# Kernel optimization log

Measured on AMD Instinct MI355X. Metric: run time of the kernel, lower is better.

## Reference

```python
import jax, jax.numpy as jnp
import numpy as np

# Sizes: B graphs, NPG nodes per graph (equal segments -> to_dense_batch == reshape),
# M instructions, DN node feat dim, DQ question dim.
B, NPG, M, DN, DQ = 64, 4096, 8, 512, 256
N = B * NPG
RATIO = 0.3
K = int(np.ceil(RATIO * NPG))  # pyg topk with ratio<1 keeps ceil(ratio*n) nodes per graph


def setup_inputs() -> dict:
    key = jax.random.key(0)
    ks = jax.random.split(key, 4)
    x = jax.random.normal(ks[0], (N, DN), jnp.float32)
    u = jax.random.normal(ks[1], (M, B, DQ), jnp.float32)
    Wn = jax.random.normal(ks[2], (DN, DQ), jnp.float32) / np.sqrt(DN)
    bn = jnp.zeros((DQ,), jnp.float32)
    batch = jnp.repeat(jnp.arange(B, dtype=jnp.int32), NPG)  # sorted graph ids, equal segments
    edge_index = jax.random.randint(ks[3], (2, 4 * N), 0, N, dtype=jnp.int32)  # unused by forward
    return {"x": x, "u": u, "Wn": Wn, "bn": bn, "batch": batch, "edge_index": edge_index}


def reference(x, u, Wn, bn, batch, edge_index):
    # node_nn: Linear(DN, DQ) + exact GELU (torch.nn.GELU default)
    h = jax.nn.gelu(x @ Wn + bn, approximate=False)            # [N, DQ]
    # to_dense_batch with equal-size graphs == reshape, mask all True
    hb = h.reshape(B, NPG, DQ)                                  # [B, n, D]
    inst = jnp.transpose(u, (1, 0, 2))                          # [B, M, D]
    scores = jnp.einsum('bmd,bnd->bmn', inst, hb)               # [B, M, n]
    attn = jax.nn.softmax(scores, axis=2)
    gate = attn.sum(axis=1)                                     # [B, n]  (gate[batch_mask] flatten)
    # per-graph ratio top-k -> hard binary mask (index_fill_ 1 at top-k, 0 elsewhere)
    kth = jax.lax.top_k(gate, K)[0][:, -1:]                     # k-th largest per graph
    mask = (gate >= kth).astype(h.dtype)                        # [B, n]
    return mask.reshape(N)
```

## Files before the change

kernel.cpp:

```cpp
#include <hip/hip_runtime.h>
#include <math.h>

#define B_     64
#define NPG_   4096
#define M_     8
#define DN_    512
#define DQ_    256
#define N_     (B_*NPG_)
#define KSEL_  1229

typedef _Float16 f16x4  __attribute__((ext_vector_type(4)));
typedef _Float16 f16x8  __attribute__((ext_vector_type(8)));
typedef float    f32x16 __attribute__((ext_vector_type(16)));

__global__ __launch_bounds__(256) void k_prep(const float* __restrict__ Wn,
                                              _Float16* __restrict__ th,
                                              _Float16* __restrict__ tl)
{
    const int k = blockIdx.x;
    const int c = threadIdx.x;
    const float w = Wn[k * DQ_ + c];
    const _Float16 h = (_Float16)w;
    th[c * DN_ + k] = h;
    tl[c * DN_ + k] = (_Float16)(w - (float)h);
}

__global__ __launch_bounds__(256, 2) void k_score(
    const float* __restrict__ x, const float* __restrict__ u,
    const float* __restrict__ bn,
    const _Float16* __restrict__ wth, const _Float16* __restrict__ wtl,
    float* __restrict__ scores)
{
    __shared__ __align__(16) _Float16 Ahi[64][40],  Alo[64][40];
    __shared__ __align__(16) _Float16 Bhi[256][40], Blo[256][40];
    __shared__ float usS[M_][DQ_];
    __shared__ float bnsS[DQ_];
    float* part4f = (float*)&Bhi[0][0];

    const int tid = threadIdx.x;
    const int ln  = tid & 63;
    const int wc  = tid >> 6;
    const int lr  = ln & 31;
    const int lh  = ln >> 5;
    const int row0 = blockIdx.x * 64;
    const int b    = row0 >> 12;

    #pragma unroll
    for (int p = 0; p < 8; ++p) {
        const int idx = p * 256 + tid;
        usS[idx >> 8][idx & 255] = u[((idx >> 8) * B_ + b) * DQ_ + (idx & 255)];
    }
    bnsS[tid] = bn[tid];

    const int arow  = tid >> 2;
    const int akoff = (tid & 3) * 8;
    const float*  xp  = x + (long)(row0 + arow) * DN_ + akoff;
    const float4* bhp = (const float4*)(wth + (long)tid * DN_);
    const float4* blp = (const float4*)(wtl + (long)tid * DN_);

    float4 xa[2], bh[4], bl[4];
    #pragma unroll
    for (int i = 0; i < 2; ++i) xa[i] = ((const float4*)xp)[i];
    #pragma unroll
    for (int j = 0; j < 4; ++j) { bh[j] = bhp[j]; bl[j] = blp[j]; }

    f32x16 acc[2][2];
    #pragma unroll
    for (int mt = 0; mt < 2; ++mt)
        #pragma unroll
        for (int nt = 0; nt < 2; ++nt)
            #pragma unroll
            for (int r = 0; r < 16; ++r) acc[mt][nt][r] = 0.0f;

    for (int kt = 0; kt < DN_ / 32; ++kt) {
        __syncthreads();

        {
            f16x8 h, l;
            h[0] = (_Float16)xa[0].x; l[0] = (_Float16)(xa[0].x - (float)h[0]);
            h[1] = (_Float16)xa[0].y; l[1] = (_Float16)(xa[0].y - (float)h[1]);
            h[2] = (_Float16)xa[0].z; l[2] = (_Float16)(xa[0].z - (float)h[2]);
            h[3] = (_Float16)xa[0].w; l[3] = (_Float16)(xa[0].w - (float)h[3]);
            h[4] = (_Float16)xa[1].x; l[4] = (_Float16)(xa[1].x - (float)h[4]);
            h[5] = (_Float16)xa[1].y; l[5] = (_Float16)(xa[1].y - (float)h[5]);
            h[6] = (_Float16)xa[1].z; l[6] = (_Float16)(xa[1].z - (float)h[6]);
            h[7] = (_Float16)xa[1].w; l[7] = (_Float16)(xa[1].w - (float)h[7]);
            *(f16x8*)&Ahi[arow][akoff] = h;
            *(f16x8*)&Alo[arow][akoff] = l;
        }
        #pragma unroll
        for (int j = 0; j < 4; ++j) {
            *(float4*)&Bhi[tid][j * 8] = bh[j];
            *(float4*)&Blo[tid][j * 8] = bl[j];
        }
        __syncthreads();

        if (kt + 1 < DN_ / 32) {
            const float* xn = xp + (kt + 1) * 32;
            #pragma unroll
            for (int i = 0; i < 2; ++i) xa[i] = ((const float4*)xn)[i];
            #pragma unroll
            for (int j = 0; j < 4; ++j) {
                bh[j] = bhp[(kt + 1) * 4 + j];
                bl[j] = blp[(kt + 1) * 4 + j];
            }
        }

        #pragma unroll
        for (int s = 0; s < 2; ++s) {
            const int o = s * 16 + lh * 8;
            f16x8 afh[2], afl[2], bfh[2], bfl[2];
            #pragma unroll
            for (int mt = 0; mt < 2; ++mt) {
                afh[mt] = *(const f16x8*)&Ahi[mt * 32 + lr][o];
                afl[mt] = *(const f16x8*)&Alo[mt * 32 + lr][o];
            }
            #pragma unroll
            for (int nt = 0; nt < 2; ++nt) {
                const int c = wc * 64 + nt * 32 + lr;
                bfh[nt] = *(const f16x8*)&Bhi[c][o];
                bfl[nt] = *(const f16x8*)&Blo[c][o];
            }
            #pragma unroll
            for (int mt = 0; mt < 2; ++mt)
                #pragma unroll
                for (int nt = 0; nt < 2; ++nt) {
                    acc[mt][nt] = __builtin_amdgcn_mfma_f32_32x32x16_f16(
                        afh[mt], bfh[nt], acc[mt][nt], 0, 0, 0);
                    acc[mt][nt] = __builtin_amdgcn_mfma_f32_32x32x16_f16(
                        afh[mt], bfl[nt], acc[mt][nt], 0, 0, 0);
                    acc[mt][nt] = __builtin_amdgcn_mfma_f32_32x32x16_f16(
                        afl[mt], bfh[nt], acc[mt][nt], 0, 0, 0);
                }
        }
    }

    #pragma unroll
    for (int mt = 0; mt < 2; ++mt)
        #pragma unroll
        for (int nt = 0; nt < 2; ++nt) {
            const float bnc = bnsS[wc * 64 + nt * 32 + lr];
            #pragma unroll
            for (int r = 0; r < 16; ++r) {
                const float z = acc[mt][nt][r] + bnc;
                acc[mt][nt][r] = 0.5f * z * (1.0f + erff(z * 0.7071067811865476f));
            }
        }

    __syncthreads();

    #pragma unroll 1
    for (int m = 0; m < 8; ++m) {
        const float u0 = usS[m][wc * 64 +  0 + lr];
        const float u1 = usS[m][wc * 64 + 32 + lr];
        float p[2][16];
        #pragma unroll
        for (int mt = 0; mt < 2; ++mt)
            #pragma unroll
            for (int r = 0; r < 16; ++r)
                p[mt][r] = acc[mt][0][r] * u0 + acc[mt][1][r] * u1;
        #pragma unroll
        for (int mask = 1; mask < 32; mask <<= 1)
            #pragma unroll
            for (int mt = 0; mt < 2; ++mt)
                #pragma unroll
                for (int r = 0; r < 16; ++r)
                    p[mt][r] += __shfl_xor(p[mt][r], mask, 64);
        if (lr == m) {
            #pragma unroll
            for (int mt = 0; mt < 2; ++mt)
                #pragma unroll
                for (int r = 0; r < 16; ++r) {
                    const int row = mt * 32 + (r & 3) + 8 * (r >> 2) + 4 * lh;
                    part4f[(wc * 64 + row) * M_ + m] = p[mt][r];
                }
        }
    }
    __syncthreads();

    #pragma unroll
    for (int i = 0; i < 2; ++i) {
        const int idx = i * 256 + tid;
        const int row = idx >> 3, m = idx & 7;
        const float v = part4f[(  0 + row) * M_ + m] + part4f[( 64 + row) * M_ + m]
                      + part4f[(128 + row) * M_ + m] + part4f[(192 + row) * M_ + m];
        scores[(long)(row0 + row) * M_ + m] = v;
    }
}

__global__ __launch_bounds__(1024) void k_mask(
    const float* __restrict__ scores, float* __restrict__ out)
{
    __shared__ float gateLDS[NPG_];
    __shared__ float wred[16][M_];
    __shared__ float gmaxS[M_];
    __shared__ float ginvS[M_];
    __shared__ unsigned hist[256];
    __shared__ unsigned sPrefix;
    __shared__ int sWant;

    const int b    = blockIdx.x;
    const int tid  = threadIdx.x;
    const int wid  = tid >> 6;
    const int lane = tid & 63;
    const float* sb = scores + (long)b * NPG_ * M_;

    float lv[8];
    #pragma unroll
    for (int m = 0; m < 8; ++m) lv[m] = -INFINITY;
    #pragma unroll
    for (int it = 0; it < 4; ++it) {
        const int n = it * 1024 + tid;
        const float4 s0 = *(const float4*)(sb + (long)n * 8);
        const float4 s1 = *(const float4*)(sb + (long)n * 8 + 4);
        lv[0] = fmaxf(lv[0], s0.x); lv[1] = fmaxf(lv[1], s0.y);
        lv[2] = fmaxf(lv[2], s0.z); lv[3] = fmaxf(lv[3], s0.w);
        lv[4] = fmaxf(lv[4], s1.x); lv[5] = fmaxf(lv[5], s1.y);
        lv[6] = fmaxf(lv[6], s1.z); lv[7] = fmaxf(lv[7], s1.w);
    }
    #pragma unroll
    for (int mask = 1; mask < 64; mask <<= 1)
        #pragma unroll
        for (int m = 0; m < 8; ++m)
            lv[m] = fmaxf(lv[m], __shfl_xor(lv[m], mask, 64));
    if (lane == 0)
        #pragma unroll
        for (int m = 0; m < 8; ++m) wred[wid][m] = lv[m];
    __syncthreads();
    if (tid < 8) {
        float mm = -INFINITY;
        for (int wv = 0; wv < 16; ++wv) mm = fmaxf(mm, wred[wv][tid]);
        gmaxS[tid] = mm;
    }
    __syncthreads();

    float gm[8];
    #pragma unroll
    for (int m = 0; m < 8; ++m) gm[m] = gmaxS[m];

    float ls[8];
    #pragma unroll
    for (int m = 0; m < 8; ++m) ls[m] = 0.0f;
    #pragma unroll
    for (int it = 0; it < 4; ++it) {
        const int n = it * 1024 + tid;
        const float4 s0 = *(const float4*)(sb + (long)n * 8);
        const float4 s1 = *(const float4*)(sb + (long)n * 8 + 4);
        ls[0] += expf(s0.x - gm[0]); ls[1] += expf(s0.y - gm[1]);
        ls[2] += expf(s0.z - gm[2]); ls[3] += expf(s0.w - gm[3]);
        ls[4] += expf(s1.x - gm[4]); ls[5] += expf(s1.y - gm[5]);
        ls[6] += expf(s1.z - gm[6]); ls[7] += expf(s1.w - gm[7]);
    }
    #pragma unroll
    for (int mask = 1; mask < 64; mask <<= 1)
        #pragma unroll
        for (int m = 0; m < 8; ++m)
            ls[m] += __shfl_xor(ls[m], mask, 64);
    if (lane == 0)
        #pragma unroll
        for (int m = 0; m < 8; ++m) wred[wid][m] = ls[m];
    __syncthreads();
    if (tid < 8) {
        float ss = 0.0f;
        for (int wv = 0; wv < 16; ++wv) ss += wred[wv][tid];
        ginvS[tid] = 1.0f / ss;
    }
    __syncthreads();

    float gi[8];
    #pragma unroll
    for (int m = 0; m < 8; ++m) gi[m] = ginvS[m];

    #pragma unroll
    for (int it = 0; it < 4; ++it) {
        const int n = it * 1024 + tid;
        const float4 s0 = *(const float4*)(sb + (long)n * 8);
        const float4 s1 = *(const float4*)(sb + (long)n * 8 + 4);
        float g = 0.0f;
        g += expf(s0.x - gm[0]) * gi[0];
        g += expf(s0.y - gm[1]) * gi[1];
        g += expf(s0.z - gm[2]) * gi[2];
        g += expf(s0.w - gm[3]) * gi[3];
        g += expf(s1.x - gm[4]) * gi[4];
        g += expf(s1.y - gm[5]) * gi[5];
        g += expf(s1.z - gm[6]) * gi[6];
        g += expf(s1.w - gm[7]) * gi[7];
        gateLDS[n] = g;
    }
    if (tid == 0) { sPrefix = 0u; sWant = KSEL_; }
    __syncthreads();

    #pragma unroll 1
    for (int r = 0; r < 4; ++r) {
        if (tid < 256) hist[tid] = 0u;
        __syncthreads();
        const unsigned pfx = sPrefix;
        const unsigned hm  = (r == 0) ? 0u :
                             (r == 1) ? 0xFF000000u :
                             (r == 2) ? 0xFFFF0000u : 0xFFFFFF00u;
        const int shift = 24 - 8 * r;
        #pragma unroll
        for (int it = 0; it < 4; ++it) {
            const unsigned uv = __float_as_uint(gateLDS[it * 1024 + tid]);
            if ((uv & hm) == pfx)
                atomicAdd(&hist[(uv >> shift) & 255u], 1u);
        }
        __syncthreads();
        if (tid == 0) {
            int want = sWant;
            unsigned acc = 0u;
            for (int bb = 255; bb >= 0; --bb) {
                const unsigned h = hist[bb];
                if (acc + h >= (unsigned)want) {
                    sWant   = want - (int)acc;
                    sPrefix = pfx | ((unsigned)bb << shift);
                    break;
                }
                acc += h;
            }
        }
        __syncthreads();
    }
    const float kth = __uint_as_float(sPrefix);

    #pragma unroll
    for (int it = 0; it < 4; ++it) {
        const int n = it * 1024 + tid;
        out[(long)b * NPG_ + n] = (gateLDS[n] >= kth) ? 1.0f : 0.0f;
    }
}

extern "C" void kernel_launch(void* const* d_in, const int* in_sizes, int n_in,
                              void* d_out, int out_size, void* d_ws, size_t ws_size,
                              hipStream_t stream) {
    const float* x  = (const float*)d_in[0];
    const float* u  = (const float*)d_in[1];
    const float* Wn = (const float*)d_in[2];
    const float* bn = (const float*)d_in[3];

    float* scores = (float*)d_ws;

    _Float16* wth = (_Float16*)d_out;
    _Float16* wtl = wth + DQ_ * DN_;
    float* out    = (float*)d_out;

    k_prep <<<DN_, 256, 0, stream>>>(Wn, wth, wtl);
    k_score<<<N_ / 64, 256, 0, stream>>>(x, u, bn, wth, wtl, scores);
    k_mask <<<B_, 1024, 0, stream>>>(scores, out);
}
```

Before: 1.394 ms.

## Load GEMM operands straight into MFMA fragments, bypassing LDS staging

```diff
diff --git a/kernel.cpp b/kernel.cpp
--- a/kernel.cpp
+++ b/kernel.cpp
@@ -9,7 +9,6 @@
 #define N_     (B_*NPG_)
 #define KSEL_  1229
 
-typedef _Float16 f16x4  __attribute__((ext_vector_type(4)));
 typedef _Float16 f16x8  __attribute__((ext_vector_type(8)));
 typedef float    f32x16 __attribute__((ext_vector_type(16)));
 
@@ -31,11 +30,9 @@
     const _Float16* __restrict__ wth, const _Float16* __restrict__ wtl,
     float* __restrict__ scores)
 {
-    __shared__ __align__(16) _Float16 Ahi[64][40],  Alo[64][40];
-    __shared__ __align__(16) _Float16 Bhi[256][40], Blo[256][40];
     __shared__ float usS[M_][DQ_];
     __shared__ float bnsS[DQ_];
-    float* part4f = (float*)&Bhi[0][0];
+    __shared__ float part4f[4 * 64 * M_];
 
     const int tid = threadIdx.x;
     const int ln  = tid & 63;
@@ -52,17 +49,68 @@
     }
     bnsS[tid] = bn[tid];
 
-    const int arow  = tid >> 2;
-    const int akoff = (tid & 3) * 8;
-    const float*  xp  = x + (long)(row0 + arow) * DN_ + akoff;
-    const float4* bhp = (const float4*)(wth + (long)tid * DN_);
-    const float4* blp = (const float4*)(wtl + (long)tid * DN_);
-
-    float4 xa[2], bh[4], bl[4];
-    #pragma unroll
-    for (int i = 0; i < 2; ++i) xa[i] = ((const float4*)xp)[i];
-    #pragma unroll
-    for (int j = 0; j < 4; ++j) { bh[j] = bhp[j]; bl[j] = blp[j]; }
+    const float* ap0 = x + (long)(row0 +  0 + lr) * DN_ + lh * 8;
+    const float* ap1 = x + (long)(row0 + 32 + lr) * DN_ + lh * 8;
+    const long c0 = (long)(wc * 64 +  0 + lr) * DN_ + lh * 8;
+    const long c1 = (long)(wc * 64 + 32 + lr) * DN_ + lh * 8;
+    const _Float16* bh0 = wth + c0;
+    const _Float16* bh1 = wth + c1;
+    const _Float16* bl0 = wtl + c0;
+    const _Float16* bl1 = wtl + c1;
+
+#define LOADK(XA, BH, BL, KT)                                           \
+    {                                                                   \
+        const int koff = (KT) * 32;                                     \
+        XA[0][0][0] = *(const float4*)(ap0 + koff +  0);                \
+        XA[0][0][1] = *(const float4*)(ap0 + koff +  4);                \
+        XA[0][1][0] = *(const float4*)(ap0 + koff + 16);                \
+        XA[0][1][1] = *(const float4*)(ap0 + koff + 20);                \
+        XA[1][0][0] = *(const float4*)(ap1 + koff +  0);                \
+        XA[1][0][1] = *(const float4*)(ap1 + koff +  4);                \
+        XA[1][1][0] = *(const float4*)(ap1 + koff + 16);                \
+        XA[1][1][1] = *(const float4*)(ap1 + koff + 20);                \
+        BH[0][0] = *(const f16x8*)(bh0 + koff);                         \
+        BH[0][1] = *(const f16x8*)(bh0 + koff + 16);                    \
+        BH[1][0] = *(const f16x8*)(bh1 + koff);                         \
+        BH[1][1] = *(const f16x8*)(bh1 + koff + 16);                    \
+        BL[0][0] = *(const f16x8*)(bl0 + koff);                         \
+        BL[0][1] = *(const f16x8*)(bl0 + koff + 16);                    \
+        BL[1][0] = *(const f16x8*)(bl1 + koff);                         \
+        BL[1][1] = *(const f16x8*)(bl1 + koff + 16);                    \
+    }
+
+#define SPLIT8(AH, AL, V0, V1)                                          \
+    AH[0] = (_Float16)V0.x; AL[0] = (_Float16)(V0.x - (float)AH[0]);    \
+    AH[1] = (_Float16)V0.y; AL[1] = (_Float16)(V0.y - (float)AH[1]);    \
+    AH[2] = (_Float16)V0.z; AL[2] = (_Float16)(V0.z - (float)AH[2]);    \
+    AH[3] = (_Float16)V0.w; AL[3] = (_Float16)(V0.w - (float)AH[3]);    \
+    AH[4] = (_Float16)V1.x; AL[4] = (_Float16)(V1.x - (float)AH[4]);    \
+    AH[5] = (_Float16)V1.y; AL[5] = (_Float16)(V1.y - (float)AH[5]);    \
+    AH[6] = (_Float16)V1.z; AL[6] = (_Float16)(V1.z - (float)AH[6]);    \
+    AH[7] = (_Float16)V1.w; AL[7] = (_Float16)(V1.w - (float)AH[7]);
+
+#define COMPUTE(XA, BH, BL)                                             \
+    _Pragma("unroll")                                                   \
+    for (int s = 0; s < 2; ++s) {                                       \
+        f16x8 ah0, al0, ah1, al1;                                       \
+        SPLIT8(ah0, al0, XA[0][s][0], XA[0][s][1]);                     \
+        SPLIT8(ah1, al1, XA[1][s][0], XA[1][s][1]);                     \
+        _Pragma("unroll")                                               \
+        for (int nt = 0; nt < 2; ++nt) {                                \
+            acc[0][nt] = __builtin_amdgcn_mfma_f32_32x32x16_f16(        \
+                ah0, BH[nt][s], acc[0][nt], 0, 0, 0);                   \
+            acc[0][nt] = __builtin_amdgcn_mfma_f32_32x32x16_f16(        \
+                ah0, BL[nt][s], acc[0][nt], 0, 0, 0);                   \
+            acc[0][nt] = __builtin_amdgcn_mfma_f32_32x32x16_f16(        \
+                al0, BH[nt][s], acc[0][nt], 0, 0, 0);                   \
+            acc[1][nt] = __builtin_amdgcn_mfma_f32_32x32x16_f16(        \
+                ah1, BH[nt][s], acc[1][nt], 0, 0, 0);                   \
+            acc[1][nt] = __builtin_amdgcn_mfma_f32_32x32x16_f16(        \
+                ah1, BL[nt][s], acc[1][nt], 0, 0, 0);                   \
+            acc[1][nt] = __builtin_amdgcn_mfma_f32_32x32x16_f16(        \
+                al1, BH[nt][s], acc[1][nt], 0, 0, 0);                   \
+        }                                                               \
+    }
 
     f32x16 acc[2][2];
     #pragma unroll
@@ -72,68 +120,19 @@
             #pragma unroll
             for (int r = 0; r < 16; ++r) acc[mt][nt][r] = 0.0f;
 
-    for (int kt = 0; kt < DN_ / 32; ++kt) {
-        __syncthreads();
-
-        {
-            f16x8 h, l;
-            h[0] = (_Float16)xa[0].x; l[0] = (_Float16)(xa[0].x - (float)h[0]);
-            h[1] = (_Float16)xa[0].y; l[1] = (_Float16)(xa[0].y - (float)h[1]);
-            h[2] = (_Float16)xa[0].z; l[2] = (_Float16)(xa[0].z - (float)h[2]);
-            h[3] = (_Float16)xa[0].w; l[3] = (_Float16)(xa[0].w - (float)h[3]);
-            h[4] = (_Float16)xa[1].x; l[4] = (_Float16)(xa[1].x - (float)h[4]);
-            h[5] = (_Float16)xa[1].y; l[5] = (_Float16)(xa[1].y - (float)h[5]);
-            h[6] = (_Float16)xa[1].z; l[6] = (_Float16)(xa[1].z - (float)h[6]);
-            h[7] = (_Float16)xa[1].w; l[7] = (_Float16)(xa[1].w - (float)h[7]);
-            *(f16x8*)&Ahi[arow][akoff] = h;
-            *(f16x8*)&Alo[arow][akoff] = l;
-        }
-        #pragma unroll
-        for (int j = 0; j < 4; ++j) {
-            *(float4*)&Bhi[tid][j * 8] = bh[j];
-            *(float4*)&Blo[tid][j * 8] = bl[j];
-        }
-        __syncthreads();
-
-        if (kt + 1 < DN_ / 32) {
-            const float* xn = xp + (kt + 1) * 32;
-            #pragma unroll
-            for (int i = 0; i < 2; ++i) xa[i] = ((const float4*)xn)[i];
-            #pragma unroll
-            for (int j = 0; j < 4; ++j) {
-                bh[j] = bhp[(kt + 1) * 4 + j];
-                bl[j] = blp[(kt + 1) * 4 + j];
-            }
-        }
-
-        #pragma unroll
-        for (int s = 0; s < 2; ++s) {
-            const int o = s * 16 + lh * 8;
-            f16x8 afh[2], afl[2], bfh[2], bfl[2];
-            #pragma unroll
-            for (int mt = 0; mt < 2; ++mt) {
-                afh[mt] = *(const f16x8*)&Ahi[mt * 32 + lr][o];
-                afl[mt] = *(const f16x8*)&Alo[mt * 32 + lr][o];
-            }
-            #pragma unroll
-            for (int nt = 0; nt < 2; ++nt) {
-                const int c = wc * 64 + nt * 32 + lr;
-                bfh[nt] = *(const f16x8*)&Bhi[c][o];
-                bfl[nt] = *(const f16x8*)&Blo[c][o];
-            }
-            #pragma unroll
-            for (int mt = 0; mt < 2; ++mt)
-                #pragma unroll
-                for (int nt = 0; nt < 2; ++nt) {
-                    acc[mt][nt] = __builtin_amdgcn_mfma_f32_32x32x16_f16(
-                        afh[mt], bfh[nt], acc[mt][nt], 0, 0, 0);
-                    acc[mt][nt] = __builtin_amdgcn_mfma_f32_32x32x16_f16(
-                        afh[mt], bfl[nt], acc[mt][nt], 0, 0, 0);
-                    acc[mt][nt] = __builtin_amdgcn_mfma_f32_32x32x16_f16(
-                        afl[mt], bfh[nt], acc[mt][nt], 0, 0, 0);
-                }
-        }
-    }
+    float4 xaA[2][2][2], xaB[2][2][2];
+    f16x8  bhA[2][2], blA[2][2], bhB[2][2], blB[2][2];
+
+    LOADK(xaA, bhA, blA, 0);
+    #pragma unroll 1
+    for (int kt = 0; kt < 16; kt += 2) {
+        LOADK(xaB, bhB, blB, kt + 1);
+        COMPUTE(xaA, bhA, blA);
+        if (kt + 2 < 16) LOADK(xaA, bhA, blA, kt + 2);
+        COMPUTE(xaB, bhB, blB);
+    }
+
+    __syncthreads();
 
     #pragma unroll
     for (int mt = 0; mt < 2; ++mt)
@@ -146,8 +145,6 @@
                 acc[mt][nt][r] = 0.5f * z * (1.0f + erff(z * 0.7071067811865476f));
             }
         }
-
-    __syncthreads();
 
     #pragma unroll 1
     for (int m = 0; m < 8; ++m) {
@@ -186,6 +183,9 @@
                       + part4f[(128 + row) * M_ + m] + part4f[(192 + row) * M_ + m];
         scores[(long)(row0 + row) * M_ + m] = v;
     }
+#undef LOADK
+#undef SPLIT8
+#undef COMPUTE
 }
 
 __global__ __launch_bounds__(1024) void k_mask(
```

After: 1.141 ms. 1.22x faster.
